# Optimization experiments

Measured on AMD Instinct MI355X. Metric: run time of the kernel, lower is better.

## Reference

```python
import jax, jax.numpy as jnp
import numpy as np

HIDDEN = 1024
HEADS = 12
HEAD_SIZE = 64
B = 8
N = 1024


def _rope(x):
    # x: [b, n, h, d] -> interleaved rotary embedding along n (seq) with last dim d
    b, n, h, d = x.shape
    inv_freq = 1.0 / (10000.0 ** (jnp.arange(0, d, 2, dtype=jnp.float32) / d))  # [d/2]
    ang = jnp.arange(n, dtype=jnp.float32)[:, None] * inv_freq[None, :]         # [n, d/2]
    cos = jnp.repeat(jnp.cos(ang), 2, axis=-1)[None, :, None, :]                # [1,n,1,d]
    sin = jnp.repeat(jnp.sin(ang), 2, axis=-1)[None, :, None, :]
    x2 = jnp.stack([-x[..., 1::2], x[..., ::2]], axis=-1).reshape(x.shape)
    return x * cos + x2 * sin


def setup_inputs() -> dict:
    key = jax.random.key(0)
    k1, k2, k3, k4 = jax.random.split(key, 4)
    inputs = jax.random.normal(k1, (B, N, HIDDEN), dtype=jnp.float32)
    mask = jax.random.randint(k2, (B, N), 0, 2, dtype=jnp.int32)
    W = jax.random.normal(k3, (HEADS * HEAD_SIZE * 2, HIDDEN), dtype=jnp.float32) * (HIDDEN ** -0.5)
    b = jax.random.normal(k4, (HEADS * HEAD_SIZE * 2,), dtype=jnp.float32) * 0.02
    return {"inputs": inputs, "mask": mask, "W": W, "b": b}


def reference(inputs, mask, W, b):
    bsz, n, _ = inputs.shape
    seq = inputs @ W.T + b                                   # [b, n, heads*2*head_size]
    seq = seq.reshape(bsz, n, HEADS, 2 * HEAD_SIZE)          # chunk+stack == reshape
    qw, kw = seq[..., :HEAD_SIZE], seq[..., HEAD_SIZE:]      # [b, n, h, d]
    qw = _rope(qw)
    kw = _rope(kw)
    logits = jnp.einsum('bmhd,bnhd->bhmn', qw, kw)           # [b, h, n, n]
    m = mask.astype(bool)
    pad = m[:, None, :, None] & m[:, None, None, :]          # valid where both positions unpadded
    logits = jnp.where(pad, logits, -jnp.inf)
    tril = jnp.tril(jnp.ones((n, n), dtype=logits.dtype), -1)
    logits = logits - tril * 1e12
    return logits / (HEAD_SIZE ** 0.5)
```

## Files before the change

### kernel.cpp

```cpp
#include <hip/hip_runtime.h>
#include <math.h>

#define HIDDEN 1024
#define HEADS 12
#define HD 64
#define BB 8
#define NN 1024
#define CC 1536

#define NEG_BIG (-1.0e30f)

typedef __attribute__((ext_vector_type(8))) short short8;
typedef __attribute__((ext_vector_type(4))) float f32x4;

__device__ __forceinline__ void async_copy16(const void* g, void* l) {
    __builtin_amdgcn_global_load_lds((const __attribute__((address_space(1))) void*)g,
                                     (__attribute__((address_space(3))) void*)l,
                                     16, 0, 0);
}

__device__ __forceinline__ unsigned short f2bf(float x) {
    union { float f; unsigned int u; } v; v.f = x;
    unsigned int r = v.u + 0x7fff + ((v.u >> 16) & 1);
    return (unsigned short)(r >> 16);
}


__global__ void rope_table_kernel(float* __restrict__ ctab, float* __restrict__ stab) {
    int idx = blockIdx.x * blockDim.x + threadIdx.x;
    if (idx >= NN * 32) return;
    int n = idx >> 5;
    int p = idx & 31;
    float inv = powf(10000.0f, -(float)p / 32.0f);
    float ang = (float)n * inv;
    ctab[idx] = cosf(ang);
    stab[idx] = sinf(ang);
}

__global__ void convert_bf16_kernel(const float* __restrict__ src,
                                    unsigned short* __restrict__ dst, int n) {
    int i = (blockIdx.x * blockDim.x + threadIdx.x) * 4;
    if (i >= n) return;
    float4 v = *(const float4*)(src + i);
    ushort4 o;
    o.x = f2bf(v.x); o.y = f2bf(v.y); o.z = f2bf(v.z); o.w = f2bf(v.w);
    *(ushort4*)(dst + i) = o;
}

__global__ __launch_bounds__(256, 3) void gemm_rope_mfma(
    const unsigned short* __restrict__ Xb,
    const unsigned short* __restrict__ Wb,
    const float* __restrict__ bias,
    const float* __restrict__ ctab, const float* __restrict__ stab,
    unsigned short* __restrict__ qout, unsigned short* __restrict__ kout)
{
    __shared__ __attribute__((aligned(16))) unsigned short As[128][64];
    __shared__ __attribute__((aligned(16))) unsigned short Bs[128][64];

    const int tid = threadIdx.x;
    const int w = tid >> 6;
    const int lane = tid & 63;
    const int m0 = blockIdx.x * 128;
    const int c0 = blockIdx.y * 128;
    const int wm = w >> 1, wn = w & 1;

    const int lrow = lane >> 3;
    const int lcol = (((lane & 7) ^ (lane >> 3)) & 7) * 8;

    f32x4 acc[4][4];
#pragma unroll
    for (int i = 0; i < 4; ++i)
#pragma unroll
        for (int j = 0; j < 4; ++j) acc[i][j] = (f32x4)(0.0f);

    for (int k0 = 0; k0 < HIDDEN; k0 += 64) {
        __syncthreads();
#pragma unroll
        for (int t = 0; t < 4; ++t) {
            int row = w * 32 + t * 8;
            async_copy16(Xb + (size_t)(m0 + row + lrow) * HIDDEN + k0 + lcol, &As[row][0]);
            async_copy16(Wb + (size_t)(c0 + row + lrow) * HIDDEN + k0 + lcol, &Bs[row][0]);
        }
        __syncthreads();

#pragma unroll
        for (int kc = 0; kc < 2; ++kc) {
            const int kg = kc * 4 + (lane >> 4);
            const int sw = ((kg ^ (lane & 7)) & 7) * 8;
            short8 a[4], b[4];
#pragma unroll
            for (int i = 0; i < 4; ++i)
                a[i] = *(const short8*)&As[wm * 64 + i * 16 + (lane & 15)][sw];
#pragma unroll
            for (int j = 0; j < 4; ++j)
                b[j] = *(const short8*)&Bs[wn * 64 + j * 16 + (lane & 15)][sw];
#pragma unroll
            for (int i = 0; i < 4; ++i)
#pragma unroll
                for (int j = 0; j < 4; ++j)
                    acc[i][j] = __builtin_amdgcn_mfma_f32_16x16x32_bf16(a[i], b[j], acc[i][j], 0, 0, 0);
        }
    }

    const int col16 = lane & 15;
    const int rquad = (lane >> 4) * 4;
    const int h = blockIdx.y;
    const bool store_lane = ((lane & 1) == 0);

#pragma unroll
    for (int j = 0; j < 4; ++j) {
        const int cl = wn * 64 + j * 16 + col16;
        const int d = cl & 63;
        const int is_k = cl >> 6;
        const int p = d >> 1;
        const float bv = bias[c0 + cl];
        unsigned short* __restrict__ outp = is_k ? kout : qout;
#pragma unroll
        for (int i = 0; i < 4; ++i) {
#pragma unroll
            for (int r = 0; r < 4; ++r) {
                const int m = m0 + wm * 64 + i * 16 + rquad + r;
                const int npos = m & (NN - 1);
                const int bidx = m >> 10;
                float v = acc[i][j][r] + bv;
                float vp = __shfl_xor(v, 1, 64);
                if (store_lane) {
                    float cs = ctab[npos * 32 + p];
                    float sn = stab[npos * 32 + p];
                    float re = v * cs - vp * sn;
                    float ro = vp * cs + v * sn;
                    unsigned int u = (unsigned int)f2bf(re) | ((unsigned int)f2bf(ro) << 16);
                    *(unsigned int*)(outp + (((size_t)(bidx * HEADS + h)) * NN + npos) * HD + d) = u;
                }
            }
        }
    }
}

__global__ __launch_bounds__(256, 3) void qk_mfma(
    const unsigned short* __restrict__ Qb,
    const unsigned short* __restrict__ Kb,
    const int* __restrict__ mask,
    float* __restrict__ out)
{
    __shared__ __attribute__((aligned(16))) unsigned short Qs[128][64];
    __shared__ __attribute__((aligned(16))) unsigned short Ks[128][64];

    const int tid = threadIdx.x;
    const int w = tid >> 6;
    const int lane = tid & 63;
    const int bh = blockIdx.z;
    const int bidx = bh / HEADS;
    const int m0 = blockIdx.y * 128;
    const int n0 = blockIdx.x * 128;
    const int wm = w >> 1, wn = w & 1;

    const unsigned short* qbase = Qb + (size_t)bh * NN * HD;
    const unsigned short* kbase = Kb + (size_t)bh * NN * HD;

    const int lrow = lane >> 3;
    const int lcol = (((lane & 7) ^ (lane >> 3)) & 7) * 8;

#pragma unroll
    for (int t = 0; t < 4; ++t) {
        int row = w * 32 + t * 8;
        async_copy16(qbase + (size_t)(m0 + row + lrow) * HD + lcol, &Qs[row][0]);
        async_copy16(kbase + (size_t)(n0 + row + lrow) * HD + lcol, &Ks[row][0]);
    }
    __syncthreads();

    f32x4 acc[4][4];
#pragma unroll
    for (int i = 0; i < 4; ++i)
#pragma unroll
        for (int j = 0; j < 4; ++j) acc[i][j] = (f32x4)(0.0f);

#pragma unroll
    for (int kc = 0; kc < 2; ++kc) {
        const int kg = kc * 4 + (lane >> 4);
        const int sw = ((kg ^ (lane & 7)) & 7) * 8;
        short8 a[4], b[4];
#pragma unroll
        for (int i = 0; i < 4; ++i)
            a[i] = *(const short8*)&Qs[wm * 64 + i * 16 + (lane & 15)][sw];
#pragma unroll
        for (int j = 0; j < 4; ++j)
            b[j] = *(const short8*)&Ks[wn * 64 + j * 16 + (lane & 15)][sw];
#pragma unroll
        for (int i = 0; i < 4; ++i)
#pragma unroll
            for (int j = 0; j < 4; ++j)
                acc[i][j] = __builtin_amdgcn_mfma_f32_16x16x32_bf16(b[j], a[i], acc[i][j], 0, 0, 0);
    }

    const int col16 = lane & 15;
    const int rquad = (lane >> 4) * 4;

    int mq[4];
#pragma unroll
    for (int i = 0; i < 4; ++i)
        mq[i] = mask[bidx * NN + m0 + wm * 64 + i * 16 + col16];

    int4 mn4[4];
#pragma unroll
    for (int j = 0; j < 4; ++j)
        mn4[j] = *(const int4*)&mask[bidx * NN + n0 + wn * 64 + j * 16 + rquad];

    float* __restrict__ obase = out + (size_t)bh * NN * NN;
#pragma unroll
    for (int i = 0; i < 4; ++i) {
        const int m = m0 + wm * 64 + i * 16 + col16;
#pragma unroll
        for (int j = 0; j < 4; ++j) {
            const int nb = n0 + wn * 64 + j * 16 + rquad;
            const int* mn = (const int*)&mn4[j];
            f32x4 t = acc[i][j];
#pragma unroll
            for (int r = 0; r < 4; ++r) {
                float v = t[r];
                if (nb + r < m) v -= 1e12f;
                v *= 0.125f;
                if (!(mq[i] && mn[r])) v = NEG_BIG;
                t[r] = v;
            }
            __builtin_nontemporal_store(t, (f32x4*)(obase + (size_t)m * NN + nb));
        }
    }
}

extern "C" void kernel_launch(void* const* d_in, const int* in_sizes, int n_in,
                              void* d_out, int out_size, void* d_ws, size_t ws_size,
                              hipStream_t stream) {
    const float* X    = (const float*)d_in[0];
    const int*   mask = (const int*)d_in[1];
    const float* W    = (const float*)d_in[2];
    const float* bias = (const float*)d_in[3];
    float* out = (float*)d_out;

    unsigned short* Xb = (unsigned short*)d_ws;
    unsigned short* Wb = Xb + (size_t)BB * NN * HIDDEN;
    unsigned short* qb = Wb + (size_t)CC * HIDDEN;
    unsigned short* kb = qb + (size_t)BB * HEADS * NN * HD;
    float* ctab = (float*)(kb + (size_t)BB * HEADS * NN * HD);
    float* stab = ctab + NN * 32;

    rope_table_kernel<<<(NN * 32 + 255) / 256, 256, 0, stream>>>(ctab, stab);

    const int nX = BB * NN * HIDDEN;
    const int nW = CC * HIDDEN;
    convert_bf16_kernel<<<(nX / 4 + 255) / 256, 256, 0, stream>>>(X, Xb, nX);
    convert_bf16_kernel<<<(nW / 4 + 255) / 256, 256, 0, stream>>>(W, Wb, nW);

    dim3 g1(BB * NN / 128, CC / 128);
    gemm_rope_mfma<<<g1, 256, 0, stream>>>(Xb, Wb, bias, ctab, stab, qb, kb);

    dim3 g2(NN / 128, NN / 128, BB * HEADS);
    qk_mfma<<<g2, 256, 0, stream>>>(qb, kb, mask, out);
}
```

Baseline: 517.5 us.

## Loop over key tiles per block with double-buffered K prefetch

Each qk block now keeps its 128-row Q tile in registers and loops over all eight 128-column K tiles, prefetching the next K tile into a second LDS buffer while computing the current one. The grid shrinks from one block per output tile to one block per (head, query tile), and the output stores switch from nontemporal to regular stores. This amortizes Q loads and launch overhead and overlaps K loads with compute. In exchange there are fewer blocks to fill the GPU (768 versus 6144), more LDS per block, and a barrier per iteration. The output write of roughly 400 MB dominates, so store efficiency matters most.

```diff
diff --git a/kernel.cpp b/kernel.cpp
--- a/kernel.cpp
+++ b/kernel.cpp
@@ -144,15 +144,14 @@
     float* __restrict__ out)
 {
     __shared__ __attribute__((aligned(16))) unsigned short Qs[128][64];
-    __shared__ __attribute__((aligned(16))) unsigned short Ks[128][64];
+    __shared__ __attribute__((aligned(16))) unsigned short Ks[2][128][64];
 
     const int tid = threadIdx.x;
     const int w = tid >> 6;
     const int lane = tid & 63;
-    const int bh = blockIdx.z;
+    const int bh = blockIdx.x;
     const int bidx = bh / HEADS;
     const int m0 = blockIdx.y * 128;
-    const int n0 = blockIdx.x * 128;
     const int wm = w >> 1, wn = w & 1;
 
     const unsigned short* qbase = Qb + (size_t)bh * NN * HD;
@@ -165,66 +164,89 @@
     for (int t = 0; t < 4; ++t) {
         int row = w * 32 + t * 8;
         async_copy16(qbase + (size_t)(m0 + row + lrow) * HD + lcol, &Qs[row][0]);
-        async_copy16(kbase + (size_t)(n0 + row + lrow) * HD + lcol, &Ks[row][0]);
+        async_copy16(kbase + (size_t)(row + lrow) * HD + lcol, &Ks[0][row][0]);
     }
     __syncthreads();
 
-    f32x4 acc[4][4];
-#pragma unroll
-    for (int i = 0; i < 4; ++i)
-#pragma unroll
-        for (int j = 0; j < 4; ++j) acc[i][j] = (f32x4)(0.0f);
-
+    const int col16 = lane & 15;
+    const int rquad = (lane >> 4) * 4;
+
+    short8 a[2][4];
 #pragma unroll
     for (int kc = 0; kc < 2; ++kc) {
         const int kg = kc * 4 + (lane >> 4);
         const int sw = ((kg ^ (lane & 7)) & 7) * 8;
-        short8 a[4], b[4];
 #pragma unroll
         for (int i = 0; i < 4; ++i)
-            a[i] = *(const short8*)&Qs[wm * 64 + i * 16 + (lane & 15)][sw];
-#pragma unroll
-        for (int j = 0; j < 4; ++j)
-            b[j] = *(const short8*)&Ks[wn * 64 + j * 16 + (lane & 15)][sw];
-#pragma unroll
-        for (int i = 0; i < 4; ++i)
-#pragma unroll
-            for (int j = 0; j < 4; ++j)
-                acc[i][j] = __builtin_amdgcn_mfma_f32_16x16x32_bf16(b[j], a[i], acc[i][j], 0, 0, 0);
-    }
-
-    const int col16 = lane & 15;
-    const int rquad = (lane >> 4) * 4;
+            a[kc][i] = *(const short8*)&Qs[wm * 64 + i * 16 + col16][sw];
+    }
 
     int mq[4];
 #pragma unroll
     for (int i = 0; i < 4; ++i)
         mq[i] = mask[bidx * NN + m0 + wm * 64 + i * 16 + col16];
 
-    int4 mn4[4];
-#pragma unroll
-    for (int j = 0; j < 4; ++j)
-        mn4[j] = *(const int4*)&mask[bidx * NN + n0 + wn * 64 + j * 16 + rquad];
-
     float* __restrict__ obase = out + (size_t)bh * NN * NN;
-#pragma unroll
-    for (int i = 0; i < 4; ++i) {
-        const int m = m0 + wm * 64 + i * 16 + col16;
-#pragma unroll
-        for (int j = 0; j < 4; ++j) {
-            const int nb = n0 + wn * 64 + j * 16 + rquad;
-            const int* mn = (const int*)&mn4[j];
-            f32x4 t = acc[i][j];
-#pragma unroll
-            for (int r = 0; r < 4; ++r) {
-                float v = t[r];
-                if (nb + r < m) v -= 1e12f;
-                v *= 0.125f;
-                if (!(mq[i] && mn[r])) v = NEG_BIG;
-                t[r] = v;
+
+    for (int nt = 0; nt < 8; ++nt) {
+        const int cur = nt & 1;
+
+        if (nt < 7) {
+#pragma unroll
+            for (int t = 0; t < 4; ++t) {
+                int row = w * 32 + t * 8;
+                async_copy16(kbase + (size_t)((nt + 1) * 128 + row + lrow) * HD + lcol,
+                             &Ks[cur ^ 1][row][0]);
             }
-            __builtin_nontemporal_store(t, (f32x4*)(obase + (size_t)m * NN + nb));
-        }
+        }
+
+        f32x4 acc[4][4];
+#pragma unroll
+        for (int i = 0; i < 4; ++i)
+#pragma unroll
+            for (int j = 0; j < 4; ++j) acc[i][j] = (f32x4)(0.0f);
+
+#pragma unroll
+        for (int kc = 0; kc < 2; ++kc) {
+            const int kg = kc * 4 + (lane >> 4);
+            const int sw = ((kg ^ (lane & 7)) & 7) * 8;
+            short8 b[4];
+#pragma unroll
+            for (int j = 0; j < 4; ++j)
+                b[j] = *(const short8*)&Ks[cur][wn * 64 + j * 16 + col16][sw];
+#pragma unroll
+            for (int i = 0; i < 4; ++i)
+#pragma unroll
+                for (int j = 0; j < 4; ++j)
+                    acc[i][j] = __builtin_amdgcn_mfma_f32_16x16x32_bf16(b[j], a[kc][i], acc[i][j], 0, 0, 0);
+        }
+
+        const int n0 = nt * 128;
+        int4 mn4[4];
+#pragma unroll
+        for (int j = 0; j < 4; ++j)
+            mn4[j] = *(const int4*)&mask[bidx * NN + n0 + wn * 64 + j * 16 + rquad];
+
+#pragma unroll
+        for (int i = 0; i < 4; ++i) {
+            const int m = m0 + wm * 64 + i * 16 + col16;
+#pragma unroll
+            for (int j = 0; j < 4; ++j) {
+                const int nb = n0 + wn * 64 + j * 16 + rquad;
+                const int* mn = (const int*)&mn4[j];
+                f32x4 t = acc[i][j];
+#pragma unroll
+                for (int r = 0; r < 4; ++r) {
+                    float v = t[r];
+                    if (nb + r < m) v -= 1e12f;
+                    v *= 0.125f;
+                    if (!(mq[i] && mn[r])) v = NEG_BIG;
+                    t[r] = v;
+                }
+                *(f32x4*)(obase + (size_t)m * NN + nb) = t;
+            }
+        }
+        __syncthreads();
     }
 }
 
@@ -254,6 +276,6 @@
     dim3 g1(BB * NN / 128, CC / 128);
     gemm_rope_mfma<<<g1, 256, 0, stream>>>(Xb, Wb, bias, ctab, stab, qb, kb);
 
-    dim3 g2(NN / 128, NN / 128, BB * HEADS);
+    dim3 g2(BB * HEADS, NN / 128);
     qk_mfma<<<g2, 256, 0, stream>>>(qb, kb, mask, out);
 }
```

Measured after the change: 591.5 us. 14.3% more time.

## Keep Q fragments in registers and loop over all key tiles per block

Applied to the files above, without the earlier changes.

The QK kernel stops staging Q and K tiles in shared memory. Each block now loads its Q fragments straight from global memory into registers once. It then loops over all eight key tiles of the row, loading K fragments directly from global memory. The grid shrinks to one block per (batch-head, m-tile), and batch-head moves to the fastest grid dimension. The aim is to drop the LDS staging and barrier, and to reuse Q across the whole output row. In exchange, K global loads are no longer swizzled or coalesced through LDS, there are fewer blocks, and the loop is serial per block.

```diff
diff --git a/kernel.cpp b/kernel.cpp
--- a/kernel.cpp
+++ b/kernel.cpp
@@ -24,7 +24,6 @@
     unsigned int r = v.u + 0x7fff + ((v.u >> 16) & 1);
     return (unsigned short)(r >> 16);
 }
-
 
 __global__ void rope_table_kernel(float* __restrict__ ctab, float* __restrict__ stab) {
     int idx = blockIdx.x * blockDim.x + threadIdx.x;
@@ -143,87 +142,85 @@
     const int* __restrict__ mask,
     float* __restrict__ out)
 {
-    __shared__ __attribute__((aligned(16))) unsigned short Qs[128][64];
-    __shared__ __attribute__((aligned(16))) unsigned short Ks[128][64];
-
     const int tid = threadIdx.x;
     const int w = tid >> 6;
     const int lane = tid & 63;
-    const int bh = blockIdx.z;
+    const int bh = blockIdx.x;
     const int bidx = bh / HEADS;
     const int m0 = blockIdx.y * 128;
-    const int n0 = blockIdx.x * 128;
     const int wm = w >> 1, wn = w & 1;
 
-    const unsigned short* qbase = Qb + (size_t)bh * NN * HD;
-    const unsigned short* kbase = Kb + (size_t)bh * NN * HD;
-
-    const int lrow = lane >> 3;
-    const int lcol = (((lane & 7) ^ (lane >> 3)) & 7) * 8;
-
-#pragma unroll
-    for (int t = 0; t < 4; ++t) {
-        int row = w * 32 + t * 8;
-        async_copy16(qbase + (size_t)(m0 + row + lrow) * HD + lcol, &Qs[row][0]);
-        async_copy16(kbase + (size_t)(n0 + row + lrow) * HD + lcol, &Ks[row][0]);
-    }
-    __syncthreads();
-
-    f32x4 acc[4][4];
-#pragma unroll
-    for (int i = 0; i < 4; ++i)
-#pragma unroll
-        for (int j = 0; j < 4; ++j) acc[i][j] = (f32x4)(0.0f);
-
+    const int col16 = lane & 15;
+    const int kgl = lane >> 4;
+    const int rquad = kgl * 4;
+
+    const unsigned short* __restrict__ qbase = Qb + (size_t)bh * NN * HD;
+    const unsigned short* __restrict__ kbase = Kb + (size_t)bh * NN * HD;
+
+    short8 a[2][4];
 #pragma unroll
     for (int kc = 0; kc < 2; ++kc) {
-        const int kg = kc * 4 + (lane >> 4);
-        const int sw = ((kg ^ (lane & 7)) & 7) * 8;
-        short8 a[4], b[4];
+        const int kg = kc * 4 + kgl;
 #pragma unroll
         for (int i = 0; i < 4; ++i)
-            a[i] = *(const short8*)&Qs[wm * 64 + i * 16 + (lane & 15)][sw];
-#pragma unroll
-        for (int j = 0; j < 4; ++j)
-            b[j] = *(const short8*)&Ks[wn * 64 + j * 16 + (lane & 15)][sw];
-#pragma unroll
-        for (int i = 0; i < 4; ++i)
-#pragma unroll
-            for (int j = 0; j < 4; ++j)
-                acc[i][j] = __builtin_amdgcn_mfma_f32_16x16x32_bf16(b[j], a[i], acc[i][j], 0, 0, 0);
-    }
-
-    const int col16 = lane & 15;
-    const int rquad = (lane >> 4) * 4;
+            a[kc][i] = *(const short8*)(qbase +
+                (size_t)(m0 + wm * 64 + i * 16 + col16) * HD + kg * 8);
+    }
 
     int mq[4];
 #pragma unroll
     for (int i = 0; i < 4; ++i)
         mq[i] = mask[bidx * NN + m0 + wm * 64 + i * 16 + col16];
 
-    int4 mn4[4];
-#pragma unroll
-    for (int j = 0; j < 4; ++j)
-        mn4[j] = *(const int4*)&mask[bidx * NN + n0 + wn * 64 + j * 16 + rquad];
-
     float* __restrict__ obase = out + (size_t)bh * NN * NN;
-#pragma unroll
-    for (int i = 0; i < 4; ++i) {
-        const int m = m0 + wm * 64 + i * 16 + col16;
-#pragma unroll
-        for (int j = 0; j < 4; ++j) {
-            const int nb = n0 + wn * 64 + j * 16 + rquad;
-            const int* mn = (const int*)&mn4[j];
-            f32x4 t = acc[i][j];
-#pragma unroll
-            for (int r = 0; r < 4; ++r) {
-                float v = t[r];
-                if (nb + r < m) v -= 1e12f;
-                v *= 0.125f;
-                if (!(mq[i] && mn[r])) v = NEG_BIG;
-                t[r] = v;
+
+    for (int nt = 0; nt < 8; ++nt) {
+        const int n0 = nt * 128;
+
+        f32x4 acc[4][4];
+#pragma unroll
+        for (int i = 0; i < 4; ++i)
+#pragma unroll
+            for (int j = 0; j < 4; ++j) acc[i][j] = (f32x4)(0.0f);
+
+#pragma unroll
+        for (int kc = 0; kc < 2; ++kc) {
+            const int kg = kc * 4 + kgl;
+            short8 b[4];
+#pragma unroll
+            for (int j = 0; j < 4; ++j)
+                b[j] = *(const short8*)(kbase +
+                    (size_t)(n0 + wn * 64 + j * 16 + col16) * HD + kg * 8);
+#pragma unroll
+            for (int i = 0; i < 4; ++i)
+#pragma unroll
+                for (int j = 0; j < 4; ++j)
+                    acc[i][j] = __builtin_amdgcn_mfma_f32_16x16x32_bf16(b[j], a[kc][i], acc[i][j], 0, 0, 0);
+        }
+
+        int4 mn4[4];
+#pragma unroll
+        for (int j = 0; j < 4; ++j)
+            mn4[j] = *(const int4*)&mask[bidx * NN + n0 + wn * 64 + j * 16 + rquad];
+
+#pragma unroll
+        for (int i = 0; i < 4; ++i) {
+            const int m = m0 + wm * 64 + i * 16 + col16;
+#pragma unroll
+            for (int j = 0; j < 4; ++j) {
+                const int nb = n0 + wn * 64 + j * 16 + rquad;
+                const int* mn = (const int*)&mn4[j];
+                f32x4 t = acc[i][j];
+#pragma unroll
+                for (int r = 0; r < 4; ++r) {
+                    float v = t[r];
+                    if (nb + r < m) v -= 1e12f;
+                    v *= 0.125f;
+                    if (!(mq[i] && mn[r])) v = NEG_BIG;
+                    t[r] = v;
+                }
+                __builtin_nontemporal_store(t, (f32x4*)(obase + (size_t)m * NN + nb));
             }
-            __builtin_nontemporal_store(t, (f32x4*)(obase + (size_t)m * NN + nb));
         }
     }
 }
@@ -254,6 +251,6 @@
     dim3 g1(BB * NN / 128, CC / 128);
     gemm_rope_mfma<<<g1, 256, 0, stream>>>(Xb, Wb, bias, ctab, stab, qb, kb);
 
-    dim3 g2(NN / 128, NN / 128, BB * HEADS);
+    dim3 g2(BB * HEADS, NN / 128);
     qk_mfma<<<g2, 256, 0, stream>>>(qb, kb, mask, out);
 }
```

Result: slower. 545.9 us (+5.5%).

## Fuse prep kernels, prefetch next GEMM tile into registers, use normal stores

Applied to the files above, without the earlier changes.

Merges the rope-table and two bf16-conversion kernels into one launch. The GEMM main loop now copies each LDS tile into registers, syncs, and immediately issues the async global-to-LDS load for the next K tile before running the MFMAs, so the load overlaps with compute. The output store in the QK kernel switches from nontemporal to a plain vector store. The cost is higher register pressure from holding two k-chunks of fragments, and possibly different cache behaviour for the large logits write.

```diff
diff --git a/kernel.cpp b/kernel.cpp
--- a/kernel.cpp
+++ b/kernel.cpp
@@ -25,26 +25,33 @@
     return (unsigned short)(r >> 16);
 }
 
-
-__global__ void rope_table_kernel(float* __restrict__ ctab, float* __restrict__ stab) {
-    int idx = blockIdx.x * blockDim.x + threadIdx.x;
-    if (idx >= NN * 32) return;
-    int n = idx >> 5;
-    int p = idx & 31;
-    float inv = powf(10000.0f, -(float)p / 32.0f);
-    float ang = (float)n * inv;
-    ctab[idx] = cosf(ang);
-    stab[idx] = sinf(ang);
-}
-
-__global__ void convert_bf16_kernel(const float* __restrict__ src,
-                                    unsigned short* __restrict__ dst, int n) {
-    int i = (blockIdx.x * blockDim.x + threadIdx.x) * 4;
-    if (i >= n) return;
-    float4 v = *(const float4*)(src + i);
-    ushort4 o;
-    o.x = f2bf(v.x); o.y = f2bf(v.y); o.z = f2bf(v.z); o.w = f2bf(v.w);
-    *(ushort4*)(dst + i) = o;
+#define NXG (BB * NN * HIDDEN / 4)
+#define NWG (CC * HIDDEN / 4)
+#define NTB (NN * 32)
+
+__global__ void prep_kernel(const float* __restrict__ X, const float* __restrict__ W,
+                            unsigned short* __restrict__ Xb, unsigned short* __restrict__ Wb,
+                            float* __restrict__ ctab, float* __restrict__ stab) {
+    int id = blockIdx.x * blockDim.x + threadIdx.x;
+    if (id < NXG + NWG) {
+        const float* src = (id < NXG) ? X : W;
+        unsigned short* dst = (id < NXG) ? Xb : Wb;
+        int i = (id < NXG) ? id : id - NXG;
+        float4 v = *(const float4*)(src + (size_t)i * 4);
+        ushort4 o;
+        o.x = f2bf(v.x); o.y = f2bf(v.y); o.z = f2bf(v.z); o.w = f2bf(v.w);
+        *(ushort4*)(dst + (size_t)i * 4) = o;
+    } else {
+        int t = id - NXG - NWG;
+        if (t < NTB) {
+            int n = t >> 5;
+            int p = t & 31;
+            float inv = powf(10000.0f, -(float)p / 32.0f);
+            float ang = (float)n * inv;
+            ctab[t] = cosf(ang);
+            stab[t] = sinf(ang);
+        }
+    }
 }
 
 __global__ __launch_bounds__(256, 3) void gemm_rope_mfma(
@@ -73,33 +80,47 @@
 #pragma unroll
         for (int j = 0; j < 4; ++j) acc[i][j] = (f32x4)(0.0f);
 
-    for (int k0 = 0; k0 < HIDDEN; k0 += 64) {
+#pragma unroll
+    for (int t = 0; t < 4; ++t) {
+        int row = w * 32 + t * 8;
+        async_copy16(Xb + (size_t)(m0 + row + lrow) * HIDDEN + lcol, &As[row][0]);
+        async_copy16(Wb + (size_t)(c0 + row + lrow) * HIDDEN + lcol, &Bs[row][0]);
+    }
+
+    for (int it = 0; it < 16; ++it) {
         __syncthreads();
-#pragma unroll
-        for (int t = 0; t < 4; ++t) {
-            int row = w * 32 + t * 8;
-            async_copy16(Xb + (size_t)(m0 + row + lrow) * HIDDEN + k0 + lcol, &As[row][0]);
-            async_copy16(Wb + (size_t)(c0 + row + lrow) * HIDDEN + k0 + lcol, &Bs[row][0]);
-        }
-        __syncthreads();
-
+
+        short8 af[2][4], bf[2][4];
 #pragma unroll
         for (int kc = 0; kc < 2; ++kc) {
             const int kg = kc * 4 + (lane >> 4);
             const int sw = ((kg ^ (lane & 7)) & 7) * 8;
-            short8 a[4], b[4];
 #pragma unroll
             for (int i = 0; i < 4; ++i)
-                a[i] = *(const short8*)&As[wm * 64 + i * 16 + (lane & 15)][sw];
+                af[kc][i] = *(const short8*)&As[wm * 64 + i * 16 + (lane & 15)][sw];
 #pragma unroll
             for (int j = 0; j < 4; ++j)
-                b[j] = *(const short8*)&Bs[wn * 64 + j * 16 + (lane & 15)][sw];
+                bf[kc][j] = *(const short8*)&Bs[wn * 64 + j * 16 + (lane & 15)][sw];
+        }
+        __syncthreads();
+
+        if (it < 15) {
+            const int k0 = (it + 1) * 64;
+#pragma unroll
+            for (int t = 0; t < 4; ++t) {
+                int row = w * 32 + t * 8;
+                async_copy16(Xb + (size_t)(m0 + row + lrow) * HIDDEN + k0 + lcol, &As[row][0]);
+                async_copy16(Wb + (size_t)(c0 + row + lrow) * HIDDEN + k0 + lcol, &Bs[row][0]);
+            }
+        }
+
+#pragma unroll
+        for (int kc = 0; kc < 2; ++kc)
 #pragma unroll
             for (int i = 0; i < 4; ++i)
 #pragma unroll
                 for (int j = 0; j < 4; ++j)
-                    acc[i][j] = __builtin_amdgcn_mfma_f32_16x16x32_bf16(a[i], b[j], acc[i][j], 0, 0, 0);
-        }
+                    acc[i][j] = __builtin_amdgcn_mfma_f32_16x16x32_bf16(af[kc][i], bf[kc][j], acc[i][j], 0, 0, 0);
     }
 
     const int col16 = lane & 15;
@@ -223,7 +244,7 @@
                 if (!(mq[i] && mn[r])) v = NEG_BIG;
                 t[r] = v;
             }
-            __builtin_nontemporal_store(t, (f32x4*)(obase + (size_t)m * NN + nb));
+            *(f32x4*)(obase + (size_t)m * NN + nb) = t;
         }
     }
 }
@@ -244,12 +265,8 @@
     float* ctab = (float*)(kb + (size_t)BB * HEADS * NN * HD);
     float* stab = ctab + NN * 32;
 
-    rope_table_kernel<<<(NN * 32 + 255) / 256, 256, 0, stream>>>(ctab, stab);
-
-    const int nX = BB * NN * HIDDEN;
-    const int nW = CC * HIDDEN;
-    convert_bf16_kernel<<<(nX / 4 + 255) / 256, 256, 0, stream>>>(X, Xb, nX);
-    convert_bf16_kernel<<<(nW / 4 + 255) / 256, 256, 0, stream>>>(W, Wb, nW);
+    const int nprep = NXG + NWG + NTB;
+    prep_kernel<<<(nprep + 255) / 256, 256, 0, stream>>>(X, W, Xb, Wb, ctab, stab);
 
     dim3 g1(BB * NN / 128, CC / 128);
     gemm_rope_mfma<<<g1, 256, 0, stream>>>(Xb, Wb, bias, ctab, stab, qb, kb);
```

New measurement: 486.8 us (median of 2 runs). 5.9% less time.
